# Kernel tuning notes

Hardware: AMD Instinct MI355X
Metric: run time of the kernel (lower is better)

## Reference

```python
import jax, jax.numpy as jnp
import numpy as np

N = 50000        # nodes
E_RAND = 800000  # random edges; self-loops appended -> E = E_RAND + N
H = 4            # heads
D_IN = 256
D_HID = 64       # per-head hidden (H*D_HID == D_IN -> identity residual in layer 1)
D_OUT = 32       # classes per head
SLOPE = 0.2      # leaky-relu negative slope


def setup_inputs() -> dict:
    key = jax.random.key(0)
    ks = jax.random.split(key, 13)
    loops = jnp.arange(N, dtype=jnp.int32)
    src = jnp.concatenate([jax.random.randint(ks[0], (E_RAND,), 0, N, dtype=jnp.int32), loops])
    dst = jnp.concatenate([jax.random.randint(ks[1], (E_RAND,), 0, N, dtype=jnp.int32), loops])
    h = jax.random.normal(ks[2], (N, D_IN), dtype=jnp.float32)
    def w(k, shape, fan):
        return jax.random.normal(k, shape, dtype=jnp.float32) * (1.0 / np.sqrt(fan))
    return {
        "h": h, "src": src, "dst": dst,
        # layer 1 (tuple in_feats -> separate fc_src / fc_dst in dgl GATConv)
        "W1_src": w(ks[3], (D_IN, H * D_HID), D_IN),
        "W1_dst": w(ks[4], (D_IN, H * D_HID), D_IN),
        "al1": w(ks[5], (H, D_HID), D_HID),
        "ar1": w(ks[6], (H, D_HID), D_HID),
        # layer 2
        "W2_src": w(ks[7], (H * D_HID, H * D_OUT), H * D_HID),
        "W2_dst": w(ks[8], (H * D_HID, H * D_OUT), H * D_HID),
        "al2": w(ks[9], (H, D_OUT), D_OUT),
        "ar2": w(ks[10], (H, D_OUT), D_OUT),
        # residual projection for layer 2 (in_dim != heads*out)
        "Wres2": w(ks[11], (H * D_HID, H * D_OUT), H * D_HID),
    }


def gat_conv(h_node, src, dst, Ws, Wd, al, ar, heads, dout, resval):
    n = h_node.shape[0]
    fs = (h_node @ Ws).reshape(n, heads, dout)   # [N,H,D] projected src feats
    fd = (h_node @ Wd).reshape(n, heads, dout)
    el = jnp.sum(fs * al, axis=-1)               # [N,H]
    er = jnp.sum(fd * ar, axis=-1)               # [N,H]
    e = jax.nn.leaky_relu(el[src] + er[dst], SLOPE)           # [E,H] edge scores
    emax = jax.ops.segment_max(e, dst, num_segments=n)        # segment softmax over dst
    ex = jnp.exp(e - emax[dst])
    denom = jax.ops.segment_sum(ex, dst, num_segments=n)
    a = ex / denom[dst]                                        # [E,H] attention
    msg = fs[src] * a[:, :, None]                              # [E,H,D] gather * weight
    out = jax.ops.segment_sum(msg, dst, num_segments=n)       # [N,H,D] scatter-add
    return out + resval


def reference(h, src, dst, W1_src, W1_dst, al1, ar1, W2_src, W2_dst, al2, ar2, Wres2):
    # layer 1: identity residual (in_dim == heads*hidden), elu activation, flatten heads
    res1 = h.reshape(-1, H, D_HID)
    h1 = gat_conv(h, src, dst, W1_src, W1_dst, al1, ar1, H, D_HID, res1)
    h1 = jax.nn.elu(h1).reshape(-1, H * D_HID)
    # layer 2: linear residual, no activation, mean over heads
    res2 = (h1 @ Wres2).reshape(-1, H, D_OUT)
    h2 = gat_conv(h1, src, dst, W2_src, W2_dst, al2, ar2, H, D_OUT, res2)
    return h2.mean(axis=1)                                     # [N, num_classes]
```

## Files before the change

### kernel.cpp

```cpp
#include <hip/hip_runtime.h>
#include <hip/hip_bf16.h>

#define NN 50000
#define EE 850000
#define NBLK_SCAN 98

typedef unsigned short u16;
using short8 = __attribute__((ext_vector_type(8))) short;
using f32x4  = __attribute__((ext_vector_type(4))) float;

__device__ __forceinline__ float bf2f(u16 u) {
    union { unsigned int i; float f; } v; v.i = ((unsigned int)u) << 16; return v.f;
}
__device__ __forceinline__ u16 f2bf(float f) {
    __hip_bfloat16 h = __float2bfloat16(f);
    return *reinterpret_cast<u16*>(&h);
}

__device__ __forceinline__ float ld1(const void* X, size_t i, bool f32m) {
    return f32m ? ((const float*)X)[i] : bf2f(((const u16*)X)[i]);
}
__device__ __forceinline__ void load4(const void* X, size_t g, bool f32m, float o[4]) {
    if (f32m) {
        float4 v = ((const float4*)X)[g];
        o[0] = v.x; o[1] = v.y; o[2] = v.z; o[3] = v.w;
    } else {
        ushort4 v = ((const ushort4*)X)[g];
        o[0] = bf2f(v.x); o[1] = bf2f(v.y); o[2] = bf2f(v.z); o[3] = bf2f(v.w);
    }
}

__global__ void k_detect(const u16* __restrict__ hh, int* __restrict__ flag,
                         int* __restrict__ deg) {
    if (blockIdx.x != 0) {
        int i = (blockIdx.x - 1) * 256 + threadIdx.x;
        if (i < NN) deg[i] = 0;
        return;
    }
    __shared__ int sm[256];
    int t = threadIdx.x;
    int c = 0;
    for (int i = 0; i < 16; ++i) {
        u16 u = hh[t * 16 + i];
        int e = (u >> 7) & 0xFF;
        if (e != 0 && (e < 90 || e > 160)) ++c;
    }
    sm[t] = c;
    __syncthreads();
    for (int s = 128; s > 0; s >>= 1) {
        if (t < s) sm[t] += sm[t + s];
        __syncthreads();
    }
    if (t == 0) *flag = (sm[0] > 200) ? 1 : 0;
}

__global__ void k_prep(const void* __restrict__ W1s, const void* __restrict__ al1,
                       const void* __restrict__ W1d, const void* __restrict__ ar1,
                       const void* __restrict__ W2s, const void* __restrict__ al2,
                       const void* __restrict__ W2d, const void* __restrict__ ar2,
                       const void* __restrict__ Wres2, const int* __restrict__ dst,
                       u16* __restrict__ BT1, u16* __restrict__ BT2,
                       float* __restrict__ wl1, float* __restrict__ wr1,
                       float* __restrict__ wl2, float* __restrict__ wr2,
                       int* __restrict__ deg, int* __restrict__ eorder,
                       const int* __restrict__ mode) {
    int bid = blockIdx.x;
    if (bid >= 528) {
        int e = (bid - 528) * 256 + threadIdx.x;
        if (e < EE) {
            int r = atomicAdd(&deg[dst[e]], 1);
            eorder[e] = r;
        }
        return;
    }
    bool f32m = (*mode) != 0;
    if (bid < 512) {
        int id = bid * 256 + threadIdx.x;
        int which = id >> 16;
        int rem = id & 65535;
        int n = rem >> 8, k = rem & 255;
        if (which == 0) {
            BT1[n * 256 + k] = f2bf(ld1(W1s, (size_t)k * 256 + n, f32m));
        } else {
            float v = (n < 128) ? ld1(W2s, (size_t)k * 128 + n, f32m)
                                : ld1(Wres2, (size_t)k * 128 + (n - 128), f32m);
            BT2[n * 256 + k] = f2bf(v);
        }
    } else {
        int id = (bid - 512) * 256 + threadIdx.x;
        int which = id >> 10;
        int rem = id & 1023;
        int k = rem >> 2, h = rem & 3;
        float s = 0.f;
        if (which == 0) {
            for (int d = 0; d < 64; ++d) s += ld1(W1s, k * 256 + h * 64 + d, f32m) * ld1(al1, h * 64 + d, f32m);
            wl1[k * 4 + h] = s;
        } else if (which == 1) {
            for (int d = 0; d < 64; ++d) s += ld1(W1d, k * 256 + h * 64 + d, f32m) * ld1(ar1, h * 64 + d, f32m);
            wr1[k * 4 + h] = s;
        } else if (which == 2) {
            for (int d = 0; d < 32; ++d) s += ld1(W2s, k * 128 + h * 32 + d, f32m) * ld1(al2, h * 32 + d, f32m);
            wl2[k * 4 + h] = s;
        } else {
            for (int d = 0; d < 32; ++d) s += ld1(W2d, k * 128 + h * 32 + d, f32m) * ld1(ar2, h * 32 + d, f32m);
            wr2[k * 4 + h] = s;
        }
    }
}

__global__ void k_scan1(const int* __restrict__ deg, int* __restrict__ rowptr,
                        int* __restrict__ bsum) {
    __shared__ int sm[512];
    int t = threadIdx.x;
    int i = blockIdx.x * 512 + t;
    int v = (i < NN) ? deg[i] : 0;
    int x = v;
    sm[t] = x;
    __syncthreads();
    for (int off = 1; off < 512; off <<= 1) {
        int y = (t >= off) ? sm[t - off] : 0;
        __syncthreads();
        x += y;
        sm[t] = x;
        __syncthreads();
    }
    if (i < NN) rowptr[i] = x - v;
    if (t == 511) bsum[blockIdx.x] = x;
}

__global__ void k_scan3_eler1(int* __restrict__ rowptr, const int* __restrict__ bsum,
                              const void* __restrict__ X,
                              const float* __restrict__ wl, const float* __restrict__ wr,
                              float* __restrict__ el, float* __restrict__ er,
                              const int* __restrict__ mode) {
    int bid = blockIdx.x;
    if (bid < 196) {
        __shared__ int sm[NBLK_SCAN];
        int t = threadIdx.x;
        if (t < NBLK_SCAN) sm[t] = bsum[t];
        __syncthreads();
        int g = bid >> 1;
        int pre = 0;
        for (int j = 0; j < g; ++j) pre += sm[j];
        int i = bid * 256 + t;
        if (i < NN) {
            rowptr[i] += pre;
            if (i == 0) rowptr[NN] = EE;
        }
        return;
    }
    bool f32m = (*mode) != 0;
    int wave = threadIdx.x >> 6, lane = threadIdx.x & 63;
    int node = (bid - 196) * 4 + wave;
    float a[4];
    load4(X, (size_t)node * 64 + lane, f32m, a);
    float accl[4] = {0, 0, 0, 0}, accr[4] = {0, 0, 0, 0};
    int k0 = lane * 4;
#pragma unroll
    for (int j = 0; j < 4; ++j) {
        float4 wlv = ((const float4*)wl)[k0 + j];
        float4 wrv = ((const float4*)wr)[k0 + j];
        accl[0] += a[j] * wlv.x; accl[1] += a[j] * wlv.y;
        accl[2] += a[j] * wlv.z; accl[3] += a[j] * wlv.w;
        accr[0] += a[j] * wrv.x; accr[1] += a[j] * wrv.y;
        accr[2] += a[j] * wrv.z; accr[3] += a[j] * wrv.w;
    }
#pragma unroll
    for (int off = 32; off > 0; off >>= 1) {
#pragma unroll
        for (int t = 0; t < 4; ++t) {
            accl[t] += __shfl_down(accl[t], off, 64);
            accr[t] += __shfl_down(accr[t], off, 64);
        }
    }
    if (lane == 0) {
        float4 vl = {accl[0], accl[1], accl[2], accl[3]};
        float4 vr = {accr[0], accr[1], accr[2], accr[3]};
        ((float4*)el)[node] = vl;
        ((float4*)er)[node] = vr;
    }
}

__global__ void k_awgen(const int* __restrict__ src, const int* __restrict__ dst,
                        const int* __restrict__ eorder, const int* __restrict__ rowptr,
                        const float* __restrict__ el, const float* __restrict__ er,
                        u16* __restrict__ aw, int* __restrict__ csrc, int writeCsrc) {
    int e = blockIdx.x * 256 + threadIdx.x;
    if (e >= EE) return;
    int s = src[e], d = dst[e];
    int slot = rowptr[d] + eorder[e];
    if (writeCsrc) csrc[slot] = s;
    float4 eL = ((const float4*)el)[s];
    float4 eR = ((const float4*)er)[d];
    float ev[4] = {eL.x + eR.x, eL.y + eR.y, eL.z + eR.z, eL.w + eR.w};
    ushort4 o;
    u16* op = (u16*)&o;
#pragma unroll
    for (int t = 0; t < 4; ++t) {
        float x = ev[t];
        x = x > 0.f ? x : 0.2f * x;
        x = fminf(fmaxf(x, -60.f), 60.f);
        op[t] = f2bf(__expf(x));
    }
    ((ushort4*)aw)[slot] = o;
}

__global__ void k_gemm_mfma(const void* __restrict__ A, int aDual,
                            const u16* __restrict__ BT, u16* __restrict__ C,
                            const int* __restrict__ mode) {
    bool af32 = aDual && ((*mode) != 0);
    __shared__ u16 At[128 * 72];
    __shared__ u16 Bt[128 * 72];
    int t = threadIdx.x;
    int lane = t & 63, w = t >> 6;
    int mt = blockIdx.x >> 1, nt = blockIdx.x & 1;
    int m0 = mt * 128, n0 = nt * 128;
    int wr = (w >> 1) * 64, wc = (w & 1) * 64;
    f32x4 acc[4][4] = {};
    int q = lane >> 4, cl = lane & 15;

    for (int ph = 0; ph < 4; ++ph) {
        int kb = ph * 64;
        for (int it = 0; it < 4; ++it) {
            int c = it * 256 + t;
            int row = c >> 3, c8 = c & 7;
            int rowg = m0 + row;
            if (af32) {
                if (rowg < NN) {
                    const float* ap = (const float*)A + (size_t)rowg * 256 + kb + c8 * 8;
                    float4 v0 = ((const float4*)ap)[0];
                    float4 v1 = ((const float4*)ap)[1];
                    ushort4 lo = {f2bf(v0.x), f2bf(v0.y), f2bf(v0.z), f2bf(v0.w)};
                    ushort4 hi = {f2bf(v1.x), f2bf(v1.y), f2bf(v1.z), f2bf(v1.w)};
                    *(ushort4*)&At[row * 72 + c8 * 8] = lo;
                    *(ushort4*)&At[row * 72 + c8 * 8 + 4] = hi;
                } else {
                    ushort4 z = {0, 0, 0, 0};
                    *(ushort4*)&At[row * 72 + c8 * 8] = z;
                    *(ushort4*)&At[row * 72 + c8 * 8 + 4] = z;
                }
            } else {
                float4 av;
                if (rowg < NN) {
                    av = *(const float4*)((const u16*)A + (size_t)rowg * 256 + kb + c8 * 8);
                } else {
                    av = make_float4(0.f, 0.f, 0.f, 0.f);
                }
                *(float4*)&At[row * 72 + c8 * 8] = av;
            }
            float4 bv = *(const float4*)(BT + (size_t)(n0 + row) * 256 + kb + c8 * 8);
            *(float4*)&Bt[row * 72 + c8 * 8] = bv;
        }
        __syncthreads();
#pragma unroll
        for (int ks = 0; ks < 2; ++ks) {
            short8 af[4], bf[4];
#pragma unroll
            for (int i = 0; i < 4; ++i)
                af[i] = *(const short8*)&At[(wr + i * 16 + cl) * 72 + ks * 32 + q * 8];
#pragma unroll
            for (int j = 0; j < 4; ++j)
                bf[j] = *(const short8*)&Bt[(wc + j * 16 + cl) * 72 + ks * 32 + q * 8];
#pragma unroll
            for (int i = 0; i < 4; ++i)
#pragma unroll
                for (int j = 0; j < 4; ++j)
                    acc[i][j] = __builtin_amdgcn_mfma_f32_16x16x32_bf16(af[i], bf[j], acc[i][j], 0, 0, 0);
        }
        __syncthreads();
    }
#pragma unroll
    for (int i = 0; i < 4; ++i)
#pragma unroll
        for (int j = 0; j < 4; ++j)
#pragma unroll
            for (int r = 0; r < 4; ++r) {
                int mrow = m0 + wr + i * 16 + q * 4 + r;
                if (mrow < NN)
                    C[(size_t)mrow * 256 + n0 + wc + j * 16 + cl] = f2bf(acc[i][j][r]);
            }
}

__global__ void k_agg1(const int* __restrict__ rowptr, const int* __restrict__ csrc,
                       const u16* __restrict__ aw, const u16* __restrict__ fs,
                       const void* __restrict__ h_in, u16* __restrict__ h1,
                       const float* __restrict__ wl2, const float* __restrict__ wr2,
                       float* __restrict__ el2, float* __restrict__ er2,
                       const int* __restrict__ mode) {
    bool f32m = (*mode) != 0;
    int wave = threadIdx.x >> 6, lane = threadIdx.x & 63;
    int node = blockIdx.x * 4 + wave;
    int beg = rowptr[node], end = rowptr[node + 1];
    int head = lane >> 4;
    float a0 = 0.f, a1 = 0.f, a2 = 0.f, a3 = 0.f, ll = 0.f;
#pragma unroll 8
    for (int p = beg; p < end; ++p) {
        int s = csrc[p];
        float pw = bf2f(aw[(size_t)p * 4 + head]);
        ushort4 fv = *(const ushort4*)(fs + (size_t)s * 256 + lane * 4);
        ll += pw;
        a0 += pw * bf2f(fv.x);
        a1 += pw * bf2f(fv.y);
        a2 += pw * bf2f(fv.z);
        a3 += pw * bf2f(fv.w);
    }
    float rinv = 1.f / ll;
    float res[4];
    load4(h_in, (size_t)node * 64 + lane, f32m, res);
    float v0 = a0 * rinv + res[0], v1 = a1 * rinv + res[1];
    float v2 = a2 * rinv + res[2], v3 = a3 * rinv + res[3];
    v0 = v0 > 0.f ? v0 : __expf(v0) - 1.f;
    v1 = v1 > 0.f ? v1 : __expf(v1) - 1.f;
    v2 = v2 > 0.f ? v2 : __expf(v2) - 1.f;
    v3 = v3 > 0.f ? v3 : __expf(v3) - 1.f;
    ushort4 o = {f2bf(v0), f2bf(v1), f2bf(v2), f2bf(v3)};
    ((ushort4*)h1)[(size_t)node * 64 + lane] = o;
    float4 w0 = ((const float4*)wl2)[lane * 4 + 0];
    float4 w1 = ((const float4*)wl2)[lane * 4 + 1];
    float4 w2 = ((const float4*)wl2)[lane * 4 + 2];
    float4 w3 = ((const float4*)wl2)[lane * 4 + 3];
    float4 r0 = ((const float4*)wr2)[lane * 4 + 0];
    float4 r1 = ((const float4*)wr2)[lane * 4 + 1];
    float4 r2 = ((const float4*)wr2)[lane * 4 + 2];
    float4 r3 = ((const float4*)wr2)[lane * 4 + 3];
    float acl[4], acr[4];
    acl[0] = v0 * w0.x + v1 * w1.x + v2 * w2.x + v3 * w3.x;
    acl[1] = v0 * w0.y + v1 * w1.y + v2 * w2.y + v3 * w3.y;
    acl[2] = v0 * w0.z + v1 * w1.z + v2 * w2.z + v3 * w3.z;
    acl[3] = v0 * w0.w + v1 * w1.w + v2 * w2.w + v3 * w3.w;
    acr[0] = v0 * r0.x + v1 * r1.x + v2 * r2.x + v3 * r3.x;
    acr[1] = v0 * r0.y + v1 * r1.y + v2 * r2.y + v3 * r3.y;
    acr[2] = v0 * r0.z + v1 * r1.z + v2 * r2.z + v3 * r3.z;
    acr[3] = v0 * r0.w + v1 * r1.w + v2 * r2.w + v3 * r3.w;
#pragma unroll
    for (int off = 32; off > 0; off >>= 1) {
#pragma unroll
        for (int t = 0; t < 4; ++t) {
            acl[t] += __shfl_down(acl[t], off, 64);
            acr[t] += __shfl_down(acr[t], off, 64);
        }
    }
    if (lane == 0) {
        float4 vl = {acl[0], acl[1], acl[2], acl[3]};
        float4 vr = {acr[0], acr[1], acr[2], acr[3]};
        ((float4*)el2)[node] = vl;
        ((float4*)er2)[node] = vr;
    }
}

__global__ void k_agg2(const int* __restrict__ rowptr, const int* __restrict__ csrc,
                       const u16* __restrict__ aw, const u16* __restrict__ c2,
                       void* __restrict__ out, const int* __restrict__ mode) {
    bool f32m = (*mode) != 0;
    int wave = threadIdx.x >> 6, lane = threadIdx.x & 63;
    int node = blockIdx.x * 4 + wave;
    int beg = rowptr[node], end = rowptr[node + 1];
    int head = lane >> 4;
    float a0 = 0.f, a1 = 0.f, ll = 0.f;
#pragma unroll 8
    for (int p = beg; p < end; ++p) {
        int s = csrc[p];
        float pw = bf2f(aw[(size_t)p * 4 + head]);
        ushort2 fv = *(const ushort2*)(c2 + (size_t)s * 256 + lane * 2);
        ll += pw;
        a0 += pw * bf2f(fv.x);
        a1 += pw * bf2f(fv.y);
    }
    float rinv = 1.f / ll;
    ushort2 rv = *(const ushort2*)(c2 + (size_t)node * 256 + 128 + lane * 2);
    float o0 = a0 * rinv + bf2f(rv.x);
    float o1 = a1 * rinv + bf2f(rv.y);
    o0 += __shfl_xor(o0, 16, 64); o0 += __shfl_xor(o0, 32, 64);
    o1 += __shfl_xor(o1, 16, 64); o1 += __shfl_xor(o1, 32, 64);
    if (lane < 16) {
        float v0 = 0.25f * o0, v1 = 0.25f * o1;
        size_t oi = (size_t)node * 32 + lane * 2;
        if (f32m) {
            ((float*)out)[oi] = v0;
            ((float*)out)[oi + 1] = v1;
        } else {
            ushort2 ov = {f2bf(v0), f2bf(v1)};
            *(ushort2*)((u16*)out + oi) = ov;
        }
    }
}

extern "C" void kernel_launch(void* const* d_in, const int* in_sizes, int n_in,
                              void* d_out, int out_size, void* d_ws, size_t ws_size,
                              hipStream_t stream) {
    int ih = 0, isrc = 1, idst = 2, iW1s = 3, iW1d = 4, ial1 = 5, iar1 = 6,
        iW2s = 7, iW2d = 8, ial2 = 9, iar2 = 10, iWres = 11;
    if (n_in >= 12 && in_sizes[0] != 12800000) {
        iW1d = 0; iW1s = 1; iW2d = 2; iW2s = 3; iWres = 4; ial1 = 5; ial2 = 6;
        iar1 = 7; iar2 = 8; idst = 9; ih = 10; isrc = 11;
    }
    const void* h     = d_in[ih];
    const int* src    = (const int*)d_in[isrc];
    const int* dst    = (const int*)d_in[idst];
    const void* W1s   = d_in[iW1s];
    const void* W1d   = d_in[iW1d];
    const void* al1   = d_in[ial1];
    const void* ar1   = d_in[iar1];
    const void* W2s   = d_in[iW2s];
    const void* W2d   = d_in[iW2d];
    const void* al2   = d_in[ial2];
    const void* ar2   = d_in[iar2];
    const void* Wres2 = d_in[iWres];

    char* w = (char*)d_ws;
    size_t off = 0;
    auto alloc = [&](size_t bytes) -> void* {
        void* p = w + off;
        off += (bytes + 255) & ~(size_t)255;
        return p;
    };
    int* mode   = (int*)alloc(256);
    float* wl1 = (float*)alloc(256 * 4 * 4);
    float* wr1 = (float*)alloc(256 * 4 * 4);
    float* wl2 = (float*)alloc(256 * 4 * 4);
    float* wr2 = (float*)alloc(256 * 4 * 4);
    int* deg    = (int*)alloc(NN * 4);
    int* rowptr = (int*)alloc((NN + 1) * 4);
    int* bsum   = (int*)alloc(NBLK_SCAN * 4);
    int* eorder = (int*)alloc((size_t)EE * 4);
    int* csrc   = (int*)alloc((size_t)EE * 4);
    u16* aw     = (u16*)alloc((size_t)EE * 4 * 2);
    float* el1  = (float*)alloc((size_t)NN * 4 * 4);
    float* er1  = (float*)alloc((size_t)NN * 4 * 4);
    float* el2  = (float*)alloc((size_t)NN * 4 * 4);
    float* er2  = (float*)alloc((size_t)NN * 4 * 4);
    u16* BT1    = (u16*)alloc(256 * 256 * 2);
    u16* BT2    = (u16*)alloc(256 * 256 * 2);
    u16* fs1    = (u16*)alloc((size_t)NN * 256 * 2);
    u16* h1     = (u16*)alloc((size_t)NN * 256 * 2);
    u16* c2     = fs1;

    k_detect<<<197, 256, 0, stream>>>((const u16*)h, mode, deg);
    k_prep<<<528 + (EE + 255) / 256, 256, 0, stream>>>(
        W1s, al1, W1d, ar1, W2s, al2, W2d, ar2, Wres2, dst,
        BT1, BT2, wl1, wr1, wl2, wr2, deg, eorder, mode);
    k_scan1<<<NBLK_SCAN, 512, 0, stream>>>(deg, rowptr, bsum);
    k_scan3_eler1<<<196 + NN / 4, 256, 0, stream>>>(rowptr, bsum,
                                                    h, wl1, wr1, el1, er1, mode);
    k_awgen<<<(EE + 255) / 256, 256, 0, stream>>>(src, dst, eorder, rowptr,
                                                  el1, er1, aw, csrc, 1);
    k_gemm_mfma<<<782, 256, 0, stream>>>(h, 1, BT1, fs1, mode);
    k_agg1<<<NN / 4, 256, 0, stream>>>(rowptr, csrc, aw, fs1, h, h1,
                                       wl2, wr2, el2, er2, mode);
    k_gemm_mfma<<<782, 256, 0, stream>>>(h1, 0, BT2, c2, mode);
    k_awgen<<<(EE + 255) / 256, 256, 0, stream>>>(src, dst, eorder, rowptr,
                                                  el2, er2, aw, csrc, 0);
    k_agg2<<<NN / 4, 256, 0, stream>>>(rowptr, csrc, aw, c2, d_out, mode);
}
```

Before: 379.1 us.

## Process multiple edges per wave with wide 16-byte gathers in aggregation kernels

Both aggregation kernels now load up to 64 edges' source indices and attention weights cooperatively per chunk and broadcast them with shuffles. Each lane then gathers 16-byte feature vectors, so the wave handles two edges per step in layer 1 and four in layer 2, with cross-lane reductions merging the partial sums. This aims to cut the serial dependent load chain of scalar index and weight loads and to widen the memory transactions. In exchange it adds shuffle overhead, more registers, and a more complex output mapping.

```diff
diff --git a/kernel.cpp b/kernel.cpp
--- a/kernel.cpp
+++ b/kernel.cpp
@@ -291,38 +291,68 @@
     int wave = threadIdx.x >> 6, lane = threadIdx.x & 63;
     int node = blockIdx.x * 4 + wave;
     int beg = rowptr[node], end = rowptr[node + 1];
-    int head = lane >> 4;
-    float a0 = 0.f, a1 = 0.f, a2 = 0.f, a3 = 0.f, ll = 0.f;
-#pragma unroll 8
-    for (int p = beg; p < end; ++p) {
-        int s = csrc[p];
-        float pw = bf2f(aw[(size_t)p * 4 + head]);
-        ushort4 fv = *(const ushort4*)(fs + (size_t)s * 256 + lane * 4);
-        ll += pw;
-        a0 += pw * bf2f(fv.x);
-        a1 += pw * bf2f(fv.y);
-        a2 += pw * bf2f(fv.z);
-        a3 += pw * bf2f(fv.w);
-    }
+    int half = lane >> 5;
+    int cl = lane & 31;
+    int head = cl >> 3;
+    uint hsel2 = head & 2, hsel1 = head & 1;
+    float acc[8] = {0, 0, 0, 0, 0, 0, 0, 0};
+    float ll = 0.f;
+    for (int cb = beg; cb < end; cb += 64) {
+        int nedge = end - cb;
+        if (nedge > 64) nedge = 64;
+        int s_l = 0;
+        uint wx_l = 0, wy_l = 0;
+        if (lane < nedge) {
+            s_l = csrc[cb + lane];
+            uint2 wv = ((const uint2*)aw)[cb + lane];
+            wx_l = wv.x; wy_l = wv.y;
+        }
+#pragma unroll 4
+        for (int j = 0; j < nedge; j += 2) {
+            int e = j + half;
+            int s = __shfl(s_l, e, 64);
+            uint wx = (uint)__shfl((int)wx_l, e, 64);
+            uint wy = (uint)__shfl((int)wy_l, e, 64);
+            uint uu = hsel2 ? wy : wx;
+            uint pb = hsel1 ? (uu & 0xffff0000u) : (uu << 16);
+            float pw = (e < nedge) ? __uint_as_float(pb) : 0.f;
+            uint4 fv = *(const uint4*)(fs + (size_t)s * 256 + cl * 8);
+            ll += pw;
+            acc[0] += pw * __uint_as_float(fv.x << 16);
+            acc[1] += pw * __uint_as_float(fv.x & 0xffff0000u);
+            acc[2] += pw * __uint_as_float(fv.y << 16);
+            acc[3] += pw * __uint_as_float(fv.y & 0xffff0000u);
+            acc[4] += pw * __uint_as_float(fv.z << 16);
+            acc[5] += pw * __uint_as_float(fv.z & 0xffff0000u);
+            acc[6] += pw * __uint_as_float(fv.w << 16);
+            acc[7] += pw * __uint_as_float(fv.w & 0xffff0000u);
+        }
+    }
+#pragma unroll
+    for (int k = 0; k < 8; ++k) acc[k] += __shfl_xor(acc[k], 32, 64);
+    ll += __shfl_xor(ll, 32, 64);
     float rinv = 1.f / ll;
+    int q = (cl << 1) | half;
     float res[4];
-    load4(h_in, (size_t)node * 64 + lane, f32m, res);
-    float v0 = a0 * rinv + res[0], v1 = a1 * rinv + res[1];
-    float v2 = a2 * rinv + res[2], v3 = a3 * rinv + res[3];
+    load4(h_in, (size_t)node * 64 + q, f32m, res);
+    float v0 = acc[half * 4 + 0] * rinv + res[0];
+    float v1 = acc[half * 4 + 1] * rinv + res[1];
+    float v2 = acc[half * 4 + 2] * rinv + res[2];
+    float v3 = acc[half * 4 + 3] * rinv + res[3];
     v0 = v0 > 0.f ? v0 : __expf(v0) - 1.f;
     v1 = v1 > 0.f ? v1 : __expf(v1) - 1.f;
     v2 = v2 > 0.f ? v2 : __expf(v2) - 1.f;
     v3 = v3 > 0.f ? v3 : __expf(v3) - 1.f;
     ushort4 o = {f2bf(v0), f2bf(v1), f2bf(v2), f2bf(v3)};
-    ((ushort4*)h1)[(size_t)node * 64 + lane] = o;
-    float4 w0 = ((const float4*)wl2)[lane * 4 + 0];
-    float4 w1 = ((const float4*)wl2)[lane * 4 + 1];
-    float4 w2 = ((const float4*)wl2)[lane * 4 + 2];
-    float4 w3 = ((const float4*)wl2)[lane * 4 + 3];
-    float4 r0 = ((const float4*)wr2)[lane * 4 + 0];
-    float4 r1 = ((const float4*)wr2)[lane * 4 + 1];
-    float4 r2 = ((const float4*)wr2)[lane * 4 + 2];
-    float4 r3 = ((const float4*)wr2)[lane * 4 + 3];
+    ((ushort4*)h1)[(size_t)node * 64 + q] = o;
+    float4 w0 = ((const float4*)wl2)[q * 4 + 0];
+    float4 w1 = ((const float4*)wl2)[q * 4 + 1];
+    float4 w2 = ((const float4*)wl2)[q * 4 + 2];
+    float4 w3 = ((const float4*)wl2)[q * 4 + 3];
+    float4 r0 = ((const float4*)wr2)[q * 4 + 0];
+    float4 r1 = ((const float4*)wr2)[q * 4 + 1];
+    float4 r2 = ((const float4*)wr2)[q * 4 + 2];
+    float4 r3 = ((const float4*)wr2)[q * 4 + 3];
     float acl[4], acr[4];
     acl[0] = v0 * w0.x + v1 * w1.x + v2 * w2.x + v3 * w3.x;
     acl[1] = v0 * w0.y + v1 * w1.y + v2 * w2.y + v3 * w3.y;
@@ -355,32 +385,79 @@
     int wave = threadIdx.x >> 6, lane = threadIdx.x & 63;
     int node = blockIdx.x * 4 + wave;
     int beg = rowptr[node], end = rowptr[node + 1];
-    int head = lane >> 4;
-    float a0 = 0.f, a1 = 0.f, ll = 0.f;
-#pragma unroll 8
-    for (int p = beg; p < end; ++p) {
-        int s = csrc[p];
-        float pw = bf2f(aw[(size_t)p * 4 + head]);
-        ushort2 fv = *(const ushort2*)(c2 + (size_t)s * 256 + lane * 2);
-        ll += pw;
-        a0 += pw * bf2f(fv.x);
-        a1 += pw * bf2f(fv.y);
-    }
+    int quarter = lane >> 4;
+    int cq = lane & 15;
+    int head = cq >> 2;
+    uint hsel2 = head & 2, hsel1 = head & 1;
+    float acc[8] = {0, 0, 0, 0, 0, 0, 0, 0};
+    float ll = 0.f;
+    for (int cb = beg; cb < end; cb += 64) {
+        int nedge = end - cb;
+        if (nedge > 64) nedge = 64;
+        int s_l = 0;
+        uint wx_l = 0, wy_l = 0;
+        if (lane < nedge) {
+            s_l = csrc[cb + lane];
+            uint2 wv = ((const uint2*)aw)[cb + lane];
+            wx_l = wv.x; wy_l = wv.y;
+        }
+#pragma unroll 2
+        for (int j = 0; j < nedge; j += 4) {
+            int e = j + quarter;
+            int s = __shfl(s_l, e, 64);
+            uint wx = (uint)__shfl((int)wx_l, e, 64);
+            uint wy = (uint)__shfl((int)wy_l, e, 64);
+            uint uu = hsel2 ? wy : wx;
+            uint pb = hsel1 ? (uu & 0xffff0000u) : (uu << 16);
+            float pw = (e < nedge) ? __uint_as_float(pb) : 0.f;
+            uint4 fv = *(const uint4*)(c2 + (size_t)s * 256 + cq * 8);
+            ll += pw;
+            acc[0] += pw * __uint_as_float(fv.x << 16);
+            acc[1] += pw * __uint_as_float(fv.x & 0xffff0000u);
+            acc[2] += pw * __uint_as_float(fv.y << 16);
+            acc[3] += pw * __uint_as_float(fv.y & 0xffff0000u);
+            acc[4] += pw * __uint_as_float(fv.z << 16);
+            acc[5] += pw * __uint_as_float(fv.z & 0xffff0000u);
+            acc[6] += pw * __uint_as_float(fv.w << 16);
+            acc[7] += pw * __uint_as_float(fv.w & 0xffff0000u);
+        }
+    }
+#pragma unroll
+    for (int k = 0; k < 8; ++k) {
+        acc[k] += __shfl_xor(acc[k], 16, 64);
+        acc[k] += __shfl_xor(acc[k], 32, 64);
+    }
+    ll += __shfl_xor(ll, 16, 64);
+    ll += __shfl_xor(ll, 32, 64);
     float rinv = 1.f / ll;
-    ushort2 rv = *(const ushort2*)(c2 + (size_t)node * 256 + 128 + lane * 2);
-    float o0 = a0 * rinv + bf2f(rv.x);
-    float o1 = a1 * rinv + bf2f(rv.y);
-    o0 += __shfl_xor(o0, 16, 64); o0 += __shfl_xor(o0, 32, 64);
-    o1 += __shfl_xor(o1, 16, 64); o1 += __shfl_xor(o1, 32, 64);
-    if (lane < 16) {
-        float v0 = 0.25f * o0, v1 = 0.25f * o1;
-        size_t oi = (size_t)node * 32 + lane * 2;
+    uint4 rv = *(const uint4*)(c2 + (size_t)node * 256 + 128 + cq * 8);
+    float m[8];
+    m[0] = acc[0] * rinv + __uint_as_float(rv.x << 16);
+    m[1] = acc[1] * rinv + __uint_as_float(rv.x & 0xffff0000u);
+    m[2] = acc[2] * rinv + __uint_as_float(rv.y << 16);
+    m[3] = acc[3] * rinv + __uint_as_float(rv.y & 0xffff0000u);
+    m[4] = acc[4] * rinv + __uint_as_float(rv.z << 16);
+    m[5] = acc[5] * rinv + __uint_as_float(rv.z & 0xffff0000u);
+    m[6] = acc[6] * rinv + __uint_as_float(rv.w << 16);
+    m[7] = acc[7] * rinv + __uint_as_float(rv.w & 0xffff0000u);
+#pragma unroll
+    for (int k = 0; k < 8; ++k) {
+        m[k] += __shfl_xor(m[k], 4, 64);
+        m[k] += __shfl_xor(m[k], 8, 64);
+        m[k] *= 0.25f;
+    }
+    if (lane < 4) {
+        size_t ob = (size_t)node * 32 + (size_t)cq * 8;
         if (f32m) {
-            ((float*)out)[oi] = v0;
-            ((float*)out)[oi + 1] = v1;
+            float4 o0 = {m[0], m[1], m[2], m[3]};
+            float4 o1 = {m[4], m[5], m[6], m[7]};
+            *(float4*)((float*)out + ob) = o0;
+            *(float4*)((float*)out + ob + 4) = o1;
         } else {
-            ushort2 ov = {f2bf(v0), f2bf(v1)};
-            *(ushort2*)((u16*)out + oi) = ov;
+            ushort4 o0 = {f2bf(m[0]), f2bf(m[1]), f2bf(m[2]), f2bf(m[3])};
+            ushort4 o1 = {f2bf(m[4]), f2bf(m[5]), f2bf(m[6]), f2bf(m[7])};
+            *(ushort4*)((u16*)out + ob) = o0;
+            *(ushort4*)((u16*)out + ob + 4) = o1;
         }
     }
 }
```

Result: no change. 381.5 us (+0.6%).

## Merge edge-weight generation into GEMM launch and use nontemporal edge loads

Applied to the files above, without the earlier changes.

The independent attention-weight kernel and the projection GEMM are combined into a single launch: blocks past the GEMM block count run the per-edge score/exp work, so both run concurrently and one launch per layer is removed. Edge index and weight streams in aggregation and awgen are read with nontemporal loads to avoid polluting cache needed for gathered features. Risks: the edge blocks now carry the GEMM's shared-memory footprint, which may lower occupancy for them, and nontemporal hints may hurt if the data was reused.

```diff
diff --git a/kernel.cpp b/kernel.cpp
--- a/kernel.cpp
+++ b/kernel.cpp
@@ -4,6 +4,7 @@
 #define NN 50000
 #define EE 850000
 #define NBLK_SCAN 98
+#define GEMM_NBLK 782
 
 typedef unsigned short u16;
 using short8 = __attribute__((ext_vector_type(8))) short;
@@ -181,36 +182,38 @@
     }
 }
 
-__global__ void k_awgen(const int* __restrict__ src, const int* __restrict__ dst,
-                        const int* __restrict__ eorder, const int* __restrict__ rowptr,
-                        const float* __restrict__ el, const float* __restrict__ er,
-                        u16* __restrict__ aw, int* __restrict__ csrc, int writeCsrc) {
-    int e = blockIdx.x * 256 + threadIdx.x;
-    if (e >= EE) return;
-    int s = src[e], d = dst[e];
-    int slot = rowptr[d] + eorder[e];
-    if (writeCsrc) csrc[slot] = s;
-    float4 eL = ((const float4*)el)[s];
-    float4 eR = ((const float4*)er)[d];
-    float ev[4] = {eL.x + eR.x, eL.y + eR.y, eL.z + eR.z, eL.w + eR.w};
-    ushort4 o;
-    u16* op = (u16*)&o;
-#pragma unroll
-    for (int t = 0; t < 4; ++t) {
-        float x = ev[t];
-        x = x > 0.f ? x : 0.2f * x;
-        x = fminf(fmaxf(x, -60.f), 60.f);
-        op[t] = f2bf(__expf(x));
-    }
-    ((ushort4*)aw)[slot] = o;
-}
-
-__global__ void k_gemm_mfma(const void* __restrict__ A, int aDual,
-                            const u16* __restrict__ BT, u16* __restrict__ C,
-                            const int* __restrict__ mode) {
-    bool af32 = aDual && ((*mode) != 0);
+__global__ void k_ga(const void* __restrict__ A, int aDual,
+                     const u16* __restrict__ BT, u16* __restrict__ C,
+                     const int* __restrict__ mode,
+                     const int* __restrict__ src, const int* __restrict__ dst,
+                     const int* __restrict__ eorder, const int* __restrict__ rowptr,
+                     const float* __restrict__ el, const float* __restrict__ er,
+                     u16* __restrict__ aw, int* __restrict__ csrc, int writeCsrc) {
     __shared__ u16 At[128 * 72];
     __shared__ u16 Bt[128 * 72];
+    if (blockIdx.x >= GEMM_NBLK) {
+        int e = (blockIdx.x - GEMM_NBLK) * 256 + threadIdx.x;
+        if (e >= EE) return;
+        int s = __builtin_nontemporal_load(&src[e]);
+        int d = __builtin_nontemporal_load(&dst[e]);
+        int slot = rowptr[d] + __builtin_nontemporal_load(&eorder[e]);
+        if (writeCsrc) csrc[slot] = s;
+        float4 eL = ((const float4*)el)[s];
+        float4 eR = ((const float4*)er)[d];
+        float ev[4] = {eL.x + eR.x, eL.y + eR.y, eL.z + eR.z, eL.w + eR.w};
+        ushort4 o;
+        u16* op = (u16*)&o;
+#pragma unroll
+        for (int t = 0; t < 4; ++t) {
+            float x = ev[t];
+            x = x > 0.f ? x : 0.2f * x;
+            x = fminf(fmaxf(x, -60.f), 60.f);
+            op[t] = f2bf(__expf(x));
+        }
+        ((ushort4*)aw)[slot] = o;
+        return;
+    }
+    bool af32 = aDual && ((*mode) != 0);
     int t = threadIdx.x;
     int lane = t & 63, w = t >> 6;
     int mt = blockIdx.x >> 1, nt = blockIdx.x & 1;
@@ -295,8 +298,8 @@
     float a0 = 0.f, a1 = 0.f, a2 = 0.f, a3 = 0.f, ll = 0.f;
 #pragma unroll 8
     for (int p = beg; p < end; ++p) {
-        int s = csrc[p];
-        float pw = bf2f(aw[(size_t)p * 4 + head]);
+        int s = __builtin_nontemporal_load(&csrc[p]);
+        float pw = bf2f(__builtin_nontemporal_load(&aw[(size_t)p * 4 + head]));
         ushort4 fv = *(const ushort4*)(fs + (size_t)s * 256 + lane * 4);
         ll += pw;
         a0 += pw * bf2f(fv.x);
@@ -359,8 +362,8 @@
     float a0 = 0.f, a1 = 0.f, ll = 0.f;
 #pragma unroll 8
     for (int p = beg; p < end; ++p) {
-        int s = csrc[p];
-        float pw = bf2f(aw[(size_t)p * 4 + head]);
+        int s = __builtin_nontemporal_load(&csrc[p]);
+        float pw = bf2f(__builtin_nontemporal_load(&aw[(size_t)p * 4 + head]));
         ushort2 fv = *(const ushort2*)(c2 + (size_t)s * 256 + lane * 2);
         ll += pw;
         a0 += pw * bf2f(fv.x);
@@ -435,20 +438,22 @@
     u16* h1     = (u16*)alloc((size_t)NN * 256 * 2);
     u16* c2     = fs1;
 
+    int awg_nblk = (EE + 255) / 256;
+
     k_detect<<<197, 256, 0, stream>>>((const u16*)h, mode, deg);
-    k_prep<<<528 + (EE + 255) / 256, 256, 0, stream>>>(
+    k_prep<<<528 + awg_nblk, 256, 0, stream>>>(
         W1s, al1, W1d, ar1, W2s, al2, W2d, ar2, Wres2, dst,
         BT1, BT2, wl1, wr1, wl2, wr2, deg, eorder, mode);
     k_scan1<<<NBLK_SCAN, 512, 0, stream>>>(deg, rowptr, bsum);
     k_scan3_eler1<<<196 + NN / 4, 256, 0, stream>>>(rowptr, bsum,
                                                     h, wl1, wr1, el1, er1, mode);
-    k_awgen<<<(EE + 255) / 256, 256, 0, stream>>>(src, dst, eorder, rowptr,
-                                                  el1, er1, aw, csrc, 1);
-    k_gemm_mfma<<<782, 256, 0, stream>>>(h, 1, BT1, fs1, mode);
+    k_ga<<<GEMM_NBLK + awg_nblk, 256, 0, stream>>>(
+        h, 1, BT1, fs1, mode,
+        src, dst, eorder, rowptr, el1, er1, aw, csrc, 1);
     k_agg1<<<NN / 4, 256, 0, stream>>>(rowptr, csrc, aw, fs1, h, h1,
                                        wl2, wr2, el2, er2, mode);
-    k_gemm_mfma<<<782, 256, 0, stream>>>(h1, 0, BT2, c2, mode);
-    k_awgen<<<(EE + 255) / 256, 256, 0, stream>>>(src, dst, eorder, rowptr,
-                                                  el2, er2, aw, csrc, 0);
+    k_ga<<<GEMM_NBLK + awg_nblk, 256, 0, stream>>>(
+        h1, 0, BT2, c2, mode,
+        src, dst, eorder, rowptr, el2, er2, aw, csrc, 0);
     k_agg2<<<NN / 4, 256, 0, stream>>>(rowptr, csrc, aw, c2, d_out, mode);
 }
```

Measured after the change: 408.5 us. +7.8%, slower.
